# Performance work log

Hardware: AMD Instinct MI355X
Metric: run time of the kernel (lower is better)

The kernel has to match this reference:

```python
import jax, jax.numpy as jnp
import numpy as np

N_NODES = 16384
N_EDGES = 65536
N_GRAPHS = 64


def setup_inputs() -> dict:
    key = jax.random.key(0)
    ks = iter(jax.random.split(key, 64))
    nk = lambda: next(ks)
    p = lambda *s: jax.random.normal(nk(), s, jnp.float32) * 0.1
    inp = {}
    inp['x'] = jax.random.normal(nk(), (N_NODES, 1), jnp.float32)
    inp['edge_index'] = jax.random.randint(nk(), (2, N_EDGES), 0, N_NODES, dtype=jnp.int32)
    inp['batch'] = jnp.sort(jax.random.randint(nk(), (N_NODES,), 0, N_GRAPHS, dtype=jnp.int32))
    for i, (fi, fo) in [(1, (1, 64)), (2, (64, 512)), (3, (512, 2048))]:
        inp[f'gat{i}_wl'] = p(fi, fo)
        inp[f'gat{i}_wr'] = p(fi, fo)
        inp[f'gat{i}_att'] = p(fo)
        inp[f'gat{i}_b'] = jnp.zeros((fo,), jnp.float32)
    for i, c in [(1, 64), (2, 512), (3, 2048), (4, 512), (5, 64)]:
        inp[f'gn{i}_w'] = jnp.ones((c,), jnp.float32)
        inp[f'gn{i}_b'] = jnp.zeros((c,), jnp.float32)
        inp[f'gn{i}_ms'] = jnp.ones((c,), jnp.float32)
    for i, (fi, fo) in [(1, (2048, 512)), (2, (512, 64))]:
        inp[f'arma{i}_wi'] = p(fi, fo)
        inp[f'arma{i}_wr'] = p(fi, fo)
        inp[f'arma{i}_b'] = jnp.zeros((fo,), jnp.float32)
    inp['lin_w'] = p(192, 2)
    inp['lin_b'] = jnp.zeros((2,), jnp.float32)
    return inp


def _seg_softmax(e, idx, n):
    m = jax.ops.segment_max(e, idx, num_segments=n)
    ex = jnp.exp(e - m[idx])
    s = jax.ops.segment_sum(ex, idx, num_segments=n)
    return ex / (s[idx] + 1e-16)


def _gatv2(x, src, dst, wl, wr, att, b):
    # GATv2: e_ij = a^T LeakyReLU(W_l x_j + W_r x_i), softmax over dst neighborhoods
    n = x.shape[0]
    xl = x @ wl
    xr = x @ wr
    e = jax.nn.leaky_relu(xl[src] + xr[dst], 0.2) @ att  # [E]
    a = _seg_softmax(e, dst, n)
    return jax.ops.segment_sum(xl[src] * a[:, None], dst, num_segments=n) + b


def _graph_norm(x, batch, w, b, ms, cnt):
    mean = jax.ops.segment_sum(x, batch, num_segments=N_GRAPHS) / cnt
    out = x - mean[batch] * ms
    var = jax.ops.segment_sum(out * out, batch, num_segments=N_GRAPHS) / cnt
    return w * out / jnp.sqrt(var + 1e-5)[batch] + b


def _arma(x, src, dst, norm, wi, wr, b):
    # ARMAConv, num_stacks=1, num_layers=1: ReLU(Ahat (x Wi) + x Wr + b)
    agg = jax.ops.segment_sum((x @ wi)[src] * norm[:, None], dst, num_segments=x.shape[0])
    return jax.nn.relu(agg + x @ wr + b)


def _forward(x, edge_index, batch,
             gat1_wl, gat1_wr, gat1_att, gat1_b, gn1_w, gn1_b, gn1_ms,
             gat2_wl, gat2_wr, gat2_att, gat2_b, gn2_w, gn2_b, gn2_ms,
             gat3_wl, gat3_wr, gat3_att, gat3_b, gn3_w, gn3_b, gn3_ms,
             arma1_wi, arma1_wr, arma1_b, gn4_w, gn4_b, gn4_ms,
             arma2_wi, arma2_wr, arma2_b, gn5_w, gn5_b, gn5_ms,
             lin_w, lin_b):
    n = x.shape[0]
    src, dst = edge_index[0], edge_index[1]
    sl = jnp.arange(n, dtype=edge_index.dtype)
    src_sl = jnp.concatenate([src, sl])  # GATv2 adds self loops
    dst_sl = jnp.concatenate([dst, sl])
    # gcn_norm without self loops (ARMAConv default)
    deg = jax.ops.segment_sum(jnp.ones_like(src, dtype=x.dtype), dst, num_segments=n)
    dis = jnp.where(deg > 0, 1.0 / jnp.sqrt(jnp.maximum(deg, 1.0)), 0.0)
    norm = dis[src] * dis[dst]
    cnt = jnp.maximum(jax.ops.segment_sum(jnp.ones((n,), x.dtype), batch, num_segments=N_GRAPHS), 1.0)[:, None]

    h = jax.nn.elu(_gatv2(x, src_sl, dst_sl, gat1_wl, gat1_wr, gat1_att, gat1_b))
    h = _graph_norm(h, batch, gn1_w, gn1_b, gn1_ms, cnt)
    h = jax.nn.elu(_gatv2(h, src_sl, dst_sl, gat2_wl, gat2_wr, gat2_att, gat2_b))
    h = _graph_norm(h, batch, gn2_w, gn2_b, gn2_ms, cnt)
    h = jax.nn.elu(_gatv2(h, src_sl, dst_sl, gat3_wl, gat3_wr, gat3_att, gat3_b))
    h = _graph_norm(h, batch, gn3_w, gn3_b, gn3_ms, cnt)
    h = jax.nn.elu(_arma(h, src, dst, norm, arma1_wi, arma1_wr, arma1_b))
    h = _graph_norm(h, batch, gn4_w, gn4_b, gn4_ms, cnt)
    h = jax.nn.elu(_arma(h, src, dst, norm, arma2_wi, arma2_wr, arma2_b))
    h = _graph_norm(h, batch, gn5_w, gn5_b, gn5_ms, cnt)

    x_max = jax.ops.segment_max(h, batch, num_segments=N_GRAPHS)
    x_sum = jax.ops.segment_sum(h, batch, num_segments=N_GRAPHS)
    x_mean = x_sum / cnt
    return jnp.concatenate([x_max, x_mean, x_sum], axis=1) @ lin_w + lin_b


def reference(x, edge_index, batch,
              gat1_wl, gat1_wr, gat1_att, gat1_b, gn1_w, gn1_b, gn1_ms,
              gat2_wl, gat2_wr, gat2_att, gat2_b, gn2_w, gn2_b, gn2_ms,
              gat3_wl, gat3_wr, gat3_att, gat3_b, gn3_w, gn3_b, gn3_ms,
              arma1_wi, arma1_wr, arma1_b, gn4_w, gn4_b, gn4_ms,
              arma2_wi, arma2_wr, arma2_b, gn5_w, gn5_b, gn5_ms,
              lin_w, lin_b):
    return _forward(x, edge_index, batch,
                    gat1_wl, gat1_wr, gat1_att, gat1_b, gn1_w, gn1_b, gn1_ms,
                    gat2_wl, gat2_wr, gat2_att, gat2_b, gn2_w, gn2_b, gn2_ms,
                    gat3_wl, gat3_wr, gat3_att, gat3_b, gn3_w, gn3_b, gn3_ms,
                    arma1_wi, arma1_wr, arma1_b, gn4_w, gn4_b, gn4_ms,
                    arma2_wi, arma2_wr, arma2_b, gn5_w, gn5_b, gn5_ms,
                    lin_w, lin_b)
```

## Files before the change

### kernel.cpp

```cpp
#include <hip/hip_runtime.h>
#include <hip/hip_bf16.h>

#define NN 16384
#define NE 65536
#define NESL (NE + NN)
#define NG 64

typedef __hip_bfloat16 bf16;
typedef __attribute__((ext_vector_type(8))) short short8v;
typedef __attribute__((ext_vector_type(4))) short short4v;
typedef __attribute__((ext_vector_type(4))) float f32x4;
typedef __attribute__((address_space(3))) void lds_void;
typedef const __attribute__((address_space(1))) void glb_void;

__device__ __forceinline__ short bfbits(float v) {
  bf16 h = __float2bfloat16(v);
  return *(short*)&h;
}
__device__ __forceinline__ float bfs2f(short s) {
  return __uint_as_float(((unsigned)(unsigned short)s) << 16);
}
__device__ __forceinline__ void gld16(const void* g, void* l) {
  __builtin_amdgcn_global_load_lds((glb_void*)g, (lds_void*)l, 16, 0, 0);
}

__global__ void k_zero2(int* a, int* b, int n) {
  int i = blockIdx.x * blockDim.x + threadIdx.x;
  if (i < n) { a[i] = 0; b[i] = 0; }
}


__global__ void k_ranges(const int* __restrict__ batch, int* __restrict__ R,
                         float* __restrict__ cnt) {
  int g = threadIdx.x;
  if (g <= NG) {
    int lo = 0, hi = NN;
    while (lo < hi) { int mid = (lo + hi) >> 1; if (batch[mid] < g) lo = mid + 1; else hi = mid; }
    R[g] = lo;
  }
  __syncthreads();
  if (g < NG) cnt[g] = fmaxf((float)(R[g + 1] - R[g]), 1.0f);
}

__global__ void k_deg(const int* __restrict__ dst, int* __restrict__ deg) {
  int e = blockIdx.x * blockDim.x + threadIdx.x;
  if (e < NE) atomicAdd(deg + dst[e], 1);
}

__global__ void k_dis(const int* __restrict__ deg, float* __restrict__ dis) {
  int n = blockIdx.x * blockDim.x + threadIdx.x;
  if (n < NN) { int d = deg[n]; dis[n] = d > 0 ? 1.0f / sqrtf((float)d) : 0.0f; }
}

__global__ void k_scan(const int* __restrict__ deg, int* __restrict__ rowptr) {
  __shared__ int sums[1024];
  int tid = threadIdx.x;
  int base = tid * 16;
  int loc[16];
  int run = 0;
#pragma unroll
  for (int i = 0; i < 16; i++) { run += deg[base + i] + 1; loc[i] = run; }
  sums[tid] = run;
  __syncthreads();
  for (int off = 1; off < 1024; off <<= 1) {
    int v = sums[tid];
    int u = (tid >= off) ? sums[tid - off] : 0;
    __syncthreads();
    sums[tid] = v + u;
    __syncthreads();
  }
  int offset = (tid > 0) ? sums[tid - 1] : 0;
  if (tid == 0) rowptr[0] = 0;
#pragma unroll
  for (int i = 0; i < 16; i++) rowptr[base + i + 1] = loc[i] + offset;
}

__global__ void k_fill(const int* __restrict__ src, const int* __restrict__ dst,
                       const int* __restrict__ rowptr, const float* __restrict__ dis,
                       int* __restrict__ fill, int* __restrict__ srck,
                       float* __restrict__ normk) {
  int e = blockIdx.x * blockDim.x + threadIdx.x;
  if (e >= NESL) return;
  int s = e < NE ? src[e] : e - NE;
  int d = e < NE ? dst[e] : e - NE;
  int pos = rowptr[d] + atomicAdd(fill + d, 1);
  srck[pos] = s;
  normk[pos] = e < NE ? dis[s] * dis[d] : 0.0f;
}

__global__ void k_wsplit2(const float* __restrict__ wa, const float* __restrict__ wb,
                          short* __restrict__ hi, short* __restrict__ lo, int K, int Nw) {
  int gi = blockIdx.x * blockDim.x + threadIdx.x;
  int ngroups = (Nw >> 6) * (K >> 5) * 512;
  if (gi >= ngroups) return;
  int g = gi & 511;
  int t = gi >> 9;
  int nkb = K >> 5;
  int tn = t / nkb, tk = t % nkb;
  int lane = g & 63;
  int n = tn * 128 + ((g >> 6) << 4) + (lane & 15);
  int kb = tk * 32 + ((lane >> 4) << 3);
  const float* w = (n < Nw) ? wa : wb;
  int nn = (n < Nw) ? n : n - Nw;
  short8v h, l;
#pragma unroll
  for (int j = 0; j < 8; j++) {
    float v = w[(size_t)(kb + j) * Nw + nn];
    short hb = bfbits(v);
    h[j] = hb;
    l[j] = bfbits(v - bfs2f(hb));
  }
  *(short8v*)(hi + (size_t)gi * 8) = h;
  *(short8v*)(lo + (size_t)gi * 8) = l;
}

template <int SPLITA, int CBF16, int ACT>
__global__ __launch_bounds__(256) void gemm_mfma_p(const short* __restrict__ Ahi,
                                                   const short* __restrict__ Alo,
                                                   const short* __restrict__ Bthi,
                                                   const short* __restrict__ Btlo,
                                                   void* __restrict__ Cp,
                                                   const float* __restrict__ bias,
                                                   int M, int N, int K) {
  __shared__ __align__(16) short sA[2][(SPLITA ? 2 : 1) * 4096];
  __shared__ __align__(16) short sB[2][8192];
  const int tid = threadIdx.x;
  const int wave = tid >> 6, lane = tid & 63;
  const int wm = wave >> 1, wn = wave & 1;
  const int nbx = gridDim.x;
  const int nwg = nbx * gridDim.y;
  const int hw = blockIdx.y * nbx + blockIdx.x;
  const int lg = (hw & 7) * (nwg >> 3) + (hw >> 3);
  const int row0 = (lg / nbx) * 128, col0 = (lg % nbx) * 128;
  const int nkb = K >> 5;
  const int c = wave * 2;
  const int ar = lane & 15, akc = lane >> 4;
  f32x4 acc[4][4] = {};

  auto stage = [&](int buf, int kb) {
    const short* bh = Bthi + ((size_t)(col0 >> 7) * nkb + kb) * 4096;
    const short* bl = Btlo + ((size_t)(col0 >> 7) * nkb + kb) * 4096;
    gld16(bh + (size_t)c * 512 + lane * 8, (char*)sB[buf] + c * 1024);
    gld16(bh + (size_t)(c + 1) * 512 + lane * 8, (char*)sB[buf] + (c + 1) * 1024);
    gld16(bl + (size_t)c * 512 + lane * 8, (char*)sB[buf] + 8192 + c * 1024);
    gld16(bl + (size_t)(c + 1) * 512 + lane * 8, (char*)sB[buf] + 8192 + (c + 1) * 1024);
    gld16(Ahi + (size_t)(row0 + c * 16 + ar) * K + kb * 32 + akc * 8,
          (char*)sA[buf] + c * 1024);
    gld16(Ahi + (size_t)(row0 + (c + 1) * 16 + ar) * K + kb * 32 + akc * 8,
          (char*)sA[buf] + (c + 1) * 1024);
    if constexpr (SPLITA) {
      gld16(Alo + (size_t)(row0 + c * 16 + ar) * K + kb * 32 + akc * 8,
            (char*)sA[buf] + 8192 + c * 1024);
      gld16(Alo + (size_t)(row0 + (c + 1) * 16 + ar) * K + kb * 32 + akc * 8,
            (char*)sA[buf] + 8192 + (c + 1) * 1024);
    }
  };

  stage(0, 0);
  for (int kb = 0; kb < nkb; kb++) {
    int cur = kb & 1;
    if (kb + 1 < nkb) {
      stage(cur ^ 1, kb + 1);
      if constexpr (SPLITA)
        asm volatile("s_waitcnt vmcnt(8)" ::: "memory");
      else
        asm volatile("s_waitcnt vmcnt(6)" ::: "memory");
    } else {
      asm volatile("s_waitcnt vmcnt(0)" ::: "memory");
    }
    __builtin_amdgcn_sched_barrier(0);
    __builtin_amdgcn_s_barrier();
    __builtin_amdgcn_sched_barrier(0);
    asm volatile("" ::: "memory");
    short8v af[4], al[4], bh[4], bl[4];
#pragma unroll
    for (int f = 0; f < 4; f++) {
      af[f] = *(short8v*)((char*)sA[cur] + (wm * 4 + f) * 1024 + lane * 16);
      if constexpr (SPLITA)
        al[f] = *(short8v*)((char*)sA[cur] + 8192 + (wm * 4 + f) * 1024 + lane * 16);
      bh[f] = *(short8v*)((char*)sB[cur] + (wn * 4 + f) * 1024 + lane * 16);
      bl[f] = *(short8v*)((char*)sB[cur] + 8192 + (wn * 4 + f) * 1024 + lane * 16);
    }
#pragma unroll
    for (int i = 0; i < 4; i++)
#pragma unroll
      for (int j = 0; j < 4; j++) {
        acc[i][j] = __builtin_amdgcn_mfma_f32_16x16x32_bf16(af[i], bh[j], acc[i][j], 0, 0, 0);
        acc[i][j] = __builtin_amdgcn_mfma_f32_16x16x32_bf16(af[i], bl[j], acc[i][j], 0, 0, 0);
        if constexpr (SPLITA)
          acc[i][j] = __builtin_amdgcn_mfma_f32_16x16x32_bf16(al[i], bh[j], acc[i][j], 0, 0, 0);
      }
    asm volatile("" ::: "memory");
    __builtin_amdgcn_sched_barrier(0);
    __builtin_amdgcn_s_barrier();
    __builtin_amdgcn_sched_barrier(0);
  }
#pragma unroll
  for (int i = 0; i < 4; i++)
#pragma unroll
    for (int j = 0; j < 4; j++)
#pragma unroll
      for (int r = 0; r < 4; r++) {
        int row = row0 + wm * 64 + i * 16 + ((lane >> 4) << 2) + r;
        int col = col0 + wn * 64 + j * 16 + (lane & 15);
        float v = acc[i][j][r];
        if (bias) v += bias[col];
        if constexpr (ACT == 1) v = v > 0.0f ? v : expf(v) - 1.0f;
        if constexpr (ACT == 2) v = fmaxf(v, 0.0f);
        if constexpr (CBF16) {
          ((short*)Cp)[(size_t)row * N + col] = bfbits(v);
        } else {
          ((float*)Cp)[(size_t)row * N + col] = v;
        }
      }
}

__global__ void k_gat1_csr(const float* __restrict__ x, const float* __restrict__ wl,
                           const float* __restrict__ wr, const float* __restrict__ att,
                           const int* __restrict__ rowptr, const int* __restrict__ srck,
                           float* __restrict__ ework, const float* __restrict__ bias,
                           float* __restrict__ out) {
  int node = blockIdx.x * 4 + (threadIdx.x >> 6);
  int lane = threadIdx.x & 63;
  float wlv = wl[lane], wrv = wr[lane], av = att[lane];
  float xd = x[node];
  int beg = rowptr[node], end = rowptr[node + 1];
  float m = -INFINITY;
  for (int k = beg; k < end; k++) {
    float v = x[srck[k]] * wlv + xd * wrv;
    v = v > 0.0f ? v : 0.2f * v;
    float e = av * v;
#pragma unroll
    for (int off = 32; off; off >>= 1) e += __shfl_xor(e, off);
    if (lane == 0) ework[k] = e;
    m = fmaxf(m, e);
  }
  __syncthreads();
  float sum = 0.0f, agg = 0.0f;
  for (int k = beg + lane; k < end; k += 64) {
    float p = expf(ework[k] - m);
    sum += p;
    agg += p * x[srck[k]];
  }
#pragma unroll
  for (int off = 32; off; off >>= 1) {
    sum += __shfl_xor(sum, off);
    agg += __shfl_xor(agg, off);
  }
  float o = agg / (sum + 1e-16f) * wlv + bias[lane];
  out[(size_t)node * 64 + lane] = o > 0.0f ? o : expf(o) - 1.0f;
}

template <int FO, int STR, typename XT>
__global__ void k_logits_csr(const XT* __restrict__ X, const float* __restrict__ att,
                             const int* __restrict__ rowptr, const int* __restrict__ srck,
                             float* __restrict__ pk, float* __restrict__ ssum) {
  int node = blockIdx.x * 4 + (threadIdx.x >> 6);
  int lane = threadIdx.x & 63;
  constexpr int NV = FO / 64;
  float xr[NV], at[NV];
  if constexpr (sizeof(XT) == 2) {
    const short* xrp = (const short*)X + (size_t)node * STR + FO;
#pragma unroll
    for (int j = 0; j < FO / 512; j++) {
      short8v v = *(const short8v*)(xrp + j * 512 + lane * 8);
      f32x4 a0 = *(const f32x4*)(att + j * 512 + lane * 8);
      f32x4 a1 = *(const f32x4*)(att + j * 512 + lane * 8 + 4);
#pragma unroll
      for (int t = 0; t < 8; t++) {
        xr[j * 8 + t] = bfs2f(v[t]);
        at[j * 8 + t] = t < 4 ? a0[t] : a1[t - 4];
      }
    }
  } else {
    const float* xrp = (const float*)X + (size_t)node * STR + FO;
#pragma unroll
    for (int j = 0; j < FO / 256; j++) {
      f32x4 v = *(const f32x4*)(xrp + j * 256 + lane * 4);
      f32x4 a = *(const f32x4*)(att + j * 256 + lane * 4);
#pragma unroll
      for (int t = 0; t < 4; t++) {
        xr[j * 4 + t] = v[t];
        at[j * 4 + t] = a[t];
      }
    }
  }
  int beg = rowptr[node], end = rowptr[node + 1];
  float m = -INFINITY;
  for (int k = beg; k < end; k++) {
    int s = srck[k];
    float acc = 0.0f;
    if constexpr (sizeof(XT) == 2) {
      const short* xlp = (const short*)X + (size_t)s * STR;
#pragma unroll
      for (int j = 0; j < FO / 512; j++) {
        short8v v = *(const short8v*)(xlp + j * 512 + lane * 8);
#pragma unroll
        for (int t = 0; t < 8; t++) {
          float u = bfs2f(v[t]) + xr[j * 8 + t];
          u = u > 0.0f ? u : 0.2f * u;
          acc += at[j * 8 + t] * u;
        }
      }
    } else {
      const float* xlp = (const float*)X + (size_t)s * STR;
#pragma unroll
      for (int j = 0; j < FO / 256; j++) {
        f32x4 v = *(const f32x4*)(xlp + j * 256 + lane * 4);
#pragma unroll
        for (int t = 0; t < 4; t++) {
          float u = v[t] + xr[j * 4 + t];
          u = u > 0.0f ? u : 0.2f * u;
          acc += at[j * 4 + t] * u;
        }
      }
    }
#pragma unroll
    for (int off = 32; off; off >>= 1) acc += __shfl_xor(acc, off);
    if (lane == 0) pk[k] = acc;
    m = fmaxf(m, acc);
  }
  __syncthreads();
  float sum = 0.0f;
  for (int k = beg + lane; k < end; k += 64) {
    float p = expf(pk[k] - m);
    pk[k] = p;
    sum += p;
  }
#pragma unroll
  for (int off = 32; off; off >>= 1) sum += __shfl_xor(sum, off);
  if (lane == 0) ssum[node] = sum;
}

template <int MODE, int SSTR, int OSTR>
__global__ void k_agg512(const float* __restrict__ Xsrc, const float* __restrict__ pk,
                         const float* __restrict__ ssum, const int* __restrict__ rowptr,
                         const int* __restrict__ srck, const float* __restrict__ normk,
                         const float* __restrict__ xwrb, const float* __restrict__ bias,
                         float* __restrict__ out, short* __restrict__ outhi,
                         short* __restrict__ outlo) {
  int wave = threadIdx.x >> 6;
  int node = blockIdx.x * 2 + (wave >> 1);
  int lane = threadIdx.x & 63;
  int c0 = (wave & 1) * 256 + lane * 4;
  f32x4 acc = {};
  int beg = rowptr[node], end = rowptr[node + 1];
  float inv = (MODE == 0) ? 1.0f / (ssum[node] + 1e-16f) : 1.0f;
  for (int k = beg; k < end; k++) {
    int s = srck[k];
    float w = (MODE == 0) ? pk[k] * inv : normk[k];
    f32x4 v = *(const f32x4*)(Xsrc + (size_t)s * SSTR + c0);
#pragma unroll
    for (int t = 0; t < 4; t++) acc[t] += w * v[t];
  }
  if constexpr (MODE == 1) {
    f32x4 xv = *(const f32x4*)(xwrb + (size_t)node * SSTR + 512 + c0);
#pragma unroll
    for (int t = 0; t < 4; t++) acc[t] = fmaxf(acc[t] + xv[t] + bias[c0 + t], 0.0f);
    *(f32x4*)(out + (size_t)node * OSTR + c0) = acc;
  } else {
    short4v hh, ll;
#pragma unroll
    for (int t = 0; t < 4; t++) {
      hh[t] = bfbits(acc[t]);
      ll[t] = bfbits(acc[t] - bfs2f(hh[t]));
    }
    *(short4v*)(outhi + (size_t)node * OSTR + c0) = hh;
    *(short4v*)(outlo + (size_t)node * OSTR + c0) = ll;
  }
}

template <int MODE, int SSTR, int XOFF>
__global__ void k_agg64(const float* __restrict__ Xsrc, const float* __restrict__ pk,
                        const float* __restrict__ ssum, const int* __restrict__ rowptr,
                        const int* __restrict__ srck, const float* __restrict__ normk,
                        const float* __restrict__ xwrb, const float* __restrict__ bias,
                        float* __restrict__ out, short* __restrict__ outhi,
                        short* __restrict__ outlo) {
  int node = blockIdx.x * (blockDim.x >> 6) + (threadIdx.x >> 6);
  if (node >= NN) return;
  int lane = threadIdx.x & 63;
  int cg = lane & 15, eg = lane >> 4;
  int c0 = cg * 4;
  f32x4 acc = {};
  int beg = rowptr[node], end = rowptr[node + 1];
  float inv = (MODE == 0) ? 1.0f / (ssum[node] + 1e-16f) : 1.0f;
  for (int k = beg + eg; k < end; k += 4) {
    int s = srck[k];
    float w = (MODE == 0) ? pk[k] * inv : normk[k];
    f32x4 v = *(const f32x4*)(Xsrc + (size_t)s * SSTR + c0);
#pragma unroll
    for (int t = 0; t < 4; t++) acc[t] += w * v[t];
  }
#pragma unroll
  for (int t = 0; t < 4; t++) {
    acc[t] += __shfl_xor(acc[t], 16);
    acc[t] += __shfl_xor(acc[t], 32);
  }
  if (eg == 0) {
    if constexpr (MODE == 1) {
      f32x4 xv = *(const f32x4*)(xwrb + (size_t)node * SSTR + XOFF + c0);
#pragma unroll
      for (int t = 0; t < 4; t++) acc[t] = fmaxf(acc[t] + xv[t] + bias[c0 + t], 0.0f);
      *(f32x4*)(out + (size_t)node * 64 + c0) = acc;
    } else {
      short4v hh, ll;
#pragma unroll
      for (int t = 0; t < 4; t++) {
        hh[t] = bfbits(acc[t]);
        ll[t] = bfbits(acc[t] - bfs2f(hh[t]));
      }
      *(short4v*)(outhi + (size_t)node * 64 + c0) = hh;
      *(short4v*)(outlo + (size_t)node * 64 + c0) = ll;
    }
  }
}

template <typename T, int VEC>
__global__ void k_gn_stats_v(const T* __restrict__ x, const int* __restrict__ R, int C,
                             float* __restrict__ s1, float* __restrict__ s2) {
  int g = blockIdx.x;
  int c0 = (blockIdx.y * blockDim.x + threadIdx.x) * VEC;
  if (c0 >= C) return;
  int beg = R[g], end = R[g + 1];
  float a[VEC] = {}, b[VEC] = {};
  for (int n = beg; n < end; n++) {
    const T* p = x + (size_t)n * C + c0;
    float v[VEC];
    if constexpr (sizeof(T) == 2) {
      short8v h = *(const short8v*)p;
#pragma unroll
      for (int t = 0; t < VEC; t++) v[t] = bfs2f(h[t]);
    } else {
      f32x4 h = *(const f32x4*)p;
#pragma unroll
      for (int t = 0; t < VEC; t++) v[t] = h[t];
    }
#pragma unroll
    for (int t = 0; t < VEC; t++) {
      a[t] += v[t];
      b[t] += v[t] * v[t];
    }
  }
#pragma unroll
  for (int t = 0; t < VEC; t++) {
    s1[g * C + c0 + t] = a[t];
    s2[g * C + c0 + t] = b[t];
  }
}

template <typename T, int VEC, int EMIT>
__global__ void k_gn_apply_v(T* __restrict__ x, const int* __restrict__ batch,
                             const float* __restrict__ cnt, const float* __restrict__ s1,
                             const float* __restrict__ s2, const float* __restrict__ w,
                             const float* __restrict__ b, const float* __restrict__ ms, int C,
                             int total_vec, short* __restrict__ hip,
                             short* __restrict__ lop) {
  int i = blockIdx.x * blockDim.x + threadIdx.x;
  if (i >= total_vec) return;
  int cpv = C / VEC;
  int n = i / cpv, c0 = (i % cpv) * VEC;
  int g = batch[n];
  float ct = cnt[g];
  T* p = x + (size_t)n * C + c0;
  float v[VEC];
  if constexpr (sizeof(T) == 2) {
    short8v h = *(const short8v*)p;
#pragma unroll
    for (int t = 0; t < VEC; t++) v[t] = bfs2f(h[t]);
  } else {
    f32x4 h = *(const f32x4*)p;
#pragma unroll
    for (int t = 0; t < VEC; t++) v[t] = h[t];
  }
#pragma unroll
  for (int t = 0; t < VEC; t++) {
    int cc = c0 + t;
    float mean = s1[g * C + cc] / ct;
    float mm = mean * ms[cc];
    float var = s2[g * C + cc] / ct - 2.0f * mm * mean + mm * mm;
    v[t] = (v[t] - mm) * (1.0f / sqrtf(var + 1e-5f)) * w[cc] + b[cc];
  }
  if constexpr (sizeof(T) == 2) {
    short8v h;
#pragma unroll
    for (int t = 0; t < VEC; t++) h[t] = bfbits(v[t]);
    *(short8v*)p = h;
  } else {
    f32x4 h;
#pragma unroll
    for (int t = 0; t < VEC; t++) h[t] = v[t];
    *(f32x4*)p = h;
  }
  if constexpr (EMIT >= 2) {
    short4v hh;
#pragma unroll
    for (int t = 0; t < VEC; t++) hh[t] = bfbits(v[t]);
    *(short4v*)(hip + (size_t)n * C + c0) = hh;
    if constexpr (EMIT == 3) {
      short4v ll;
#pragma unroll
      for (int t = 0; t < VEC; t++) ll[t] = bfbits(v[t] - bfs2f(hh[t]));
      *(short4v*)(lop + (size_t)n * C + c0) = ll;
    }
  }
}

__global__ void k_pool(const float* __restrict__ h, const int* __restrict__ R,
                       const float* __restrict__ cnt, const float* __restrict__ lw,
                       const float* __restrict__ lb, float* __restrict__ out) {
  int g = blockIdx.x;
  int c = threadIdx.x;
  int beg = R[g], end = R[g + 1];
  float mx = -INFINITY, sm = 0.0f;
  for (int n = beg; n < end; n++) {
    float v = h[(size_t)n * 64 + c];
    mx = fmaxf(mx, v);
    sm += v;
  }
  __shared__ float feat[192];
  feat[c] = mx;
  feat[64 + c] = sm / cnt[g];
  feat[128 + c] = sm;
  __syncthreads();
  if (c < 2) {
    float acc = lb[c];
    for (int j = 0; j < 192; j++) acc += feat[j] * lw[j * 2 + c];
    out[g * 2 + c] = acc;
  }
}


extern "C" void kernel_launch(void* const* d_in, const int* in_sizes, int n_in,
                              void* d_out, int out_size, void* d_ws, size_t ws_size,
                              hipStream_t stream) {
  const float* x = (const float*)d_in[0];
  const int* ei = (const int*)d_in[1];
  const int* batch = (const int*)d_in[2];
  const float* g1wl = (const float*)d_in[3];
  const float* g1wr = (const float*)d_in[4];
  const float* g1att = (const float*)d_in[5];
  const float* g1b = (const float*)d_in[6];
  const float* g2wl = (const float*)d_in[7];
  const float* g2wr = (const float*)d_in[8];
  const float* g2att = (const float*)d_in[9];
  const float* g2b = (const float*)d_in[10];
  const float* g3wl = (const float*)d_in[11];
  const float* g3wr = (const float*)d_in[12];
  const float* g3att = (const float*)d_in[13];
  const float* g3b = (const float*)d_in[14];
  const float* gn1w = (const float*)d_in[15];
  const float* gn1b = (const float*)d_in[16];
  const float* gn1ms = (const float*)d_in[17];
  const float* gn2w = (const float*)d_in[18];
  const float* gn2b = (const float*)d_in[19];
  const float* gn2ms = (const float*)d_in[20];
  const float* gn3w = (const float*)d_in[21];
  const float* gn3b = (const float*)d_in[22];
  const float* gn3ms = (const float*)d_in[23];
  const float* gn4w = (const float*)d_in[24];
  const float* gn4b = (const float*)d_in[25];
  const float* gn4ms = (const float*)d_in[26];
  const float* gn5w = (const float*)d_in[27];
  const float* gn5b = (const float*)d_in[28];
  const float* gn5ms = (const float*)d_in[29];
  const float* a1wi = (const float*)d_in[30];
  const float* a1wr = (const float*)d_in[31];
  const float* a1b = (const float*)d_in[32];
  const float* a2wi = (const float*)d_in[33];
  const float* a2wr = (const float*)d_in[34];
  const float* a2b = (const float*)d_in[35];
  const float* linw = (const float*)d_in[36];
  const float* linb = (const float*)d_in[37];
  const int* srcp = ei;
  const int* dstp = ei + NE;
  float* out = (float*)d_out;

  float* ws = (float*)d_ws;
  size_t o = 0;
  auto alloc = [&](size_t nfloats) { float* p = ws + o; o += nfloats; return p; };
  float* BIG0f = alloc((size_t)NN * 1024);
  float* BIG1f = alloc((size_t)NN * 1024);
  float* B0 = alloc((size_t)NN * 512);
  float* B1 = alloc((size_t)NN * 512);
  float* h1 = alloc((size_t)NN * 64);
  float* S0 = alloc((size_t)NN * 64);
  float* S1 = alloc((size_t)NN * 64);
  float* S2 = alloc((size_t)NN * 64);
  float* pk = alloc(NESL);
  float* normk = alloc(NESL);
  float* ssum = alloc(NN);
  float* dis = alloc(NN);
  float* cnt = alloc(NG);
  float* s1 = alloc(NG * 2048);
  float* s2 = alloc(NG * 2048);
  short* WThi = (short*)alloc((size_t)4096 * 512 / 2);
  short* WTlo = (short*)alloc((size_t)4096 * 512 / 2);
  int* deg = (int*)alloc(NN);
  int* rowptr = (int*)alloc(NN + 1);
  int* fill = (int*)alloc(NN);
  int* srck = (int*)alloc(NESL);
  int* R = (int*)alloc(72);

  bf16* XLR3 = (bf16*)BIG0f;
  bf16* h3 = (bf16*)BIG0f;
  float* h4 = BIG1f;
  short* h4hi = (short*)BIG0f;
  short* h4lo = h4hi + (size_t)NN * 512;
  short* XLR2 = (short*)B0;
  float* h2 = B0;
  short* h2hi = (short*)B1;
  short* agg2hi = (short*)B1;
  short* agg2lo = agg2hi + (size_t)NN * 512;
  float* TXW1 = B0;
  float* TXW2 = S0;
  short* h1hi = (short*)S2;
  short* h1lo = h1hi + (size_t)NN * 64;
  short* aggShi = (short*)S0;
  short* aggSlo = aggShi + (size_t)NN * 64;
  float* h5 = S2;

  k_zero2<<<NN / 256, 256, 0, stream>>>(deg, fill, NN);
  k_ranges<<<1, 128, 0, stream>>>(batch, R, cnt);
  k_deg<<<NE / 256, 256, 0, stream>>>(dstp, deg);
  k_scan<<<1, 1024, 0, stream>>>(deg, rowptr);
  k_dis<<<NN / 256, 256, 0, stream>>>(deg, dis);
  k_fill<<<(NESL + 255) / 256, 256, 0, stream>>>(srcp, dstp, rowptr, dis, fill, srck, normk);

  k_gat1_csr<<<NN / 4, 256, 0, stream>>>(x, g1wl, g1wr, g1att, rowptr, srck, pk, g1b, h1);
  k_gn_stats_v<float, 4><<<dim3(NG, 1), 16, 0, stream>>>(h1, R, 64, s1, s2);
  k_gn_apply_v<float, 4, 3><<<NN * 16 / 256, 256, 0, stream>>>(h1, batch, cnt, s1, s2, gn1w,
                                                               gn1b, gn1ms, 64, NN * 16, h1hi,
                                                               h1lo);

  k_wsplit2<<<8192 / 256, 256, 0, stream>>>(g2wl, g2wr, WThi, WTlo, 64, 512);
  gemm_mfma_p<1, 1, 0><<<dim3(8, 128), 256, 0, stream>>>(h1hi, h1lo, WThi, WTlo, XLR2, nullptr,
                                                         NN, 1024, 64);
  k_logits_csr<512, 1024, bf16><<<NN / 4, 256, 0, stream>>>((const bf16*)XLR2, g2att, rowptr,
                                                            srck, pk, ssum);
  k_agg64<0, 64, 0><<<NN / 4, 256, 0, stream>>>(h1, pk, ssum, rowptr, srck, normk, nullptr,
                                                nullptr, nullptr, aggShi, aggSlo);
  gemm_mfma_p<1, 0, 1><<<dim3(4, 128), 256, 0, stream>>>(aggShi, aggSlo, WThi, WTlo, h2, g2b,
                                                         NN, 512, 64);
  k_gn_stats_v<float, 4><<<dim3(NG, 1), 128, 0, stream>>>(h2, R, 512, s1, s2);
  k_gn_apply_v<float, 4, 2><<<NN * 128 / 256, 256, 0, stream>>>(h2, batch, cnt, s1, s2, gn2w,
                                                                gn2b, gn2ms, 512, NN * 128,
                                                                h2hi, nullptr);

  k_wsplit2<<<262144 / 256, 256, 0, stream>>>(g3wl, g3wr, WThi, WTlo, 512, 2048);
  gemm_mfma_p<0, 1, 0><<<dim3(32, 128), 256, 0, stream>>>(h2hi, nullptr, WThi, WTlo, XLR3,
                                                          nullptr, NN, 4096, 512);
  k_logits_csr<2048, 4096, bf16><<<NN / 4, 256, 0, stream>>>(XLR3, g3att, rowptr, srck, pk, ssum);
  k_agg512<0, 512, 512><<<NN / 2, 256, 0, stream>>>(h2, pk, ssum, rowptr, srck, normk, nullptr,
                                                    nullptr, nullptr, agg2hi, agg2lo);
  gemm_mfma_p<1, 1, 1><<<dim3(16, 128), 256, 0, stream>>>(agg2hi, agg2lo, WThi, WTlo, h3, g3b,
                                                          NN, 2048, 512);
  k_gn_stats_v<bf16, 8><<<dim3(NG, 1), 256, 0, stream>>>(h3, R, 2048, s1, s2);
  k_gn_apply_v<bf16, 8, 0><<<NN * 256 / 256, 256, 0, stream>>>(h3, batch, cnt, s1, s2, gn3w,
                                                               gn3b, gn3ms, 2048, NN * 256,
                                                               nullptr, nullptr);

  k_wsplit2<<<262144 / 256, 256, 0, stream>>>(a1wi, a1wr, WThi, WTlo, 2048, 512);
  gemm_mfma_p<0, 0, 0><<<dim3(8, 128), 256, 0, stream>>>((const short*)h3, nullptr, WThi, WTlo,
                                                         TXW1, nullptr, NN, 1024, 2048);
  k_agg512<1, 1024, 512><<<NN / 2, 256, 0, stream>>>(TXW1, pk, nullptr, rowptr, srck, normk,
                                                     TXW1, a1b, h4, nullptr, nullptr);
  k_gn_stats_v<float, 4><<<dim3(NG, 1), 128, 0, stream>>>(h4, R, 512, s1, s2);
  k_gn_apply_v<float, 4, 3><<<NN * 128 / 256, 256, 0, stream>>>(h4, batch, cnt, s1, s2, gn4w,
                                                                gn4b, gn4ms, 512, NN * 128,
                                                                h4hi, h4lo);

  k_wsplit2<<<8192 / 256, 256, 0, stream>>>(a2wi, a2wr, WThi, WTlo, 512, 64);
  gemm_mfma_p<1, 0, 0><<<dim3(1, 128), 256, 0, stream>>>(h4hi, h4lo, WThi, WTlo, TXW2, nullptr,
                                                         NN, 128, 512);
  k_agg64<1, 128, 64><<<NN / 4, 256, 0, stream>>>(TXW2, pk, nullptr, rowptr, srck, normk, TXW2,
                                                  a2b, h5, nullptr, nullptr);
  k_gn_stats_v<float, 4><<<dim3(NG, 1), 16, 0, stream>>>(h5, R, 64, s1, s2);
  k_gn_apply_v<float, 4, 0><<<NN * 16 / 256, 256, 0, stream>>>(h5, batch, cnt, s1, s2, gn5w,
                                                               gn5b, gn5ms, 64, NN * 16, nullptr,
                                                               nullptr);

  k_pool<<<NG, 64, 0, stream>>>(h5, R, cnt, linw, linb, out);
}
```

Measured before the change: 1.279 ms.

## Add 256-row GEMM tile variant and split graph-norm stats over row chunks

```diff
diff --git a/kernel.cpp b/kernel.cpp
--- a/kernel.cpp
+++ b/kernel.cpp
@@ -215,6 +215,98 @@
       }
 }
 
+template <int CBF16, int ACT>
+__global__ __launch_bounds__(512) void gemm_mfma_p256(const short* __restrict__ Ahi,
+                                                      const short* __restrict__ Bthi,
+                                                      const short* __restrict__ Btlo,
+                                                      void* __restrict__ Cp,
+                                                      const float* __restrict__ bias,
+                                                      int M, int N, int K) {
+  __shared__ __align__(16) short sA[2][8192];
+  __shared__ __align__(16) short sB[2][8192];
+  const int tid = threadIdx.x;
+  const int wave = tid >> 6, lane = tid & 63;
+  const int wm = wave >> 1, wn = wave & 1;
+  const int nbx = gridDim.x;
+  const int nwg = nbx * gridDim.y;
+  const int hw = blockIdx.y * nbx + blockIdx.x;
+  const int lg = (hw & 7) * (nwg >> 3) + (hw >> 3);
+  const int row0 = (lg / nbx) * 256, col0 = (lg % nbx) * 128;
+  const int nkb = K >> 5;
+  const int ar = lane & 15, akc = lane >> 4;
+  f32x4 acc[4][4] = {};
+
+  auto stage = [&](int buf, int kb) {
+    if (wave < 4) {
+      const short* bh = Bthi + ((size_t)(col0 >> 7) * nkb + kb) * 4096;
+      int cB = wave * 2;
+      gld16(bh + (size_t)cB * 512 + lane * 8, (char*)sB[buf] + cB * 1024);
+      gld16(bh + (size_t)(cB + 1) * 512 + lane * 8, (char*)sB[buf] + (cB + 1) * 1024);
+    } else {
+      const short* bl = Btlo + ((size_t)(col0 >> 7) * nkb + kb) * 4096;
+      int cB = (wave - 4) * 2;
+      gld16(bl + (size_t)cB * 512 + lane * 8, (char*)sB[buf] + 8192 + cB * 1024);
+      gld16(bl + (size_t)(cB + 1) * 512 + lane * 8, (char*)sB[buf] + 8192 + (cB + 1) * 1024);
+    }
+    int cA = wave * 2;
+    gld16(Ahi + (size_t)(row0 + cA * 16 + ar) * K + kb * 32 + akc * 8,
+          (char*)sA[buf] + cA * 1024);
+    gld16(Ahi + (size_t)(row0 + (cA + 1) * 16 + ar) * K + kb * 32 + akc * 8,
+          (char*)sA[buf] + (cA + 1) * 1024);
+  };
+
+  stage(0, 0);
+  for (int kb = 0; kb < nkb; kb++) {
+    int cur = kb & 1;
+    if (kb + 1 < nkb) {
+      stage(cur ^ 1, kb + 1);
+      asm volatile("s_waitcnt vmcnt(4)" ::: "memory");
+    } else {
+      asm volatile("s_waitcnt vmcnt(0)" ::: "memory");
+    }
+    __builtin_amdgcn_sched_barrier(0);
+    __builtin_amdgcn_s_barrier();
+    __builtin_amdgcn_sched_barrier(0);
+    asm volatile("" ::: "memory");
+    short8v af[4], bh[4], bl[4];
+#pragma unroll
+    for (int f = 0; f < 4; f++) {
+      af[f] = *(short8v*)((char*)sA[cur] + (wm * 4 + f) * 1024 + lane * 16);
+      bh[f] = *(short8v*)((char*)sB[cur] + (wn * 4 + f) * 1024 + lane * 16);
+      bl[f] = *(short8v*)((char*)sB[cur] + 8192 + (wn * 4 + f) * 1024 + lane * 16);
+    }
+#pragma unroll
+    for (int i = 0; i < 4; i++)
+#pragma unroll
+      for (int j = 0; j < 4; j++) {
+        acc[i][j] = __builtin_amdgcn_mfma_f32_16x16x32_bf16(af[i], bh[j], acc[i][j], 0, 0, 0);
+        acc[i][j] = __builtin_amdgcn_mfma_f32_16x16x32_bf16(af[i], bl[j], acc[i][j], 0, 0, 0);
+      }
+    asm volatile("" ::: "memory");
+    __builtin_amdgcn_sched_barrier(0);
+    __builtin_amdgcn_s_barrier();
+    __builtin_amdgcn_sched_barrier(0);
+  }
+#pragma unroll
+  for (int i = 0; i < 4; i++)
+#pragma unroll
+    for (int j = 0; j < 4; j++)
+#pragma unroll
+      for (int r = 0; r < 4; r++) {
+        int row = row0 + wm * 64 + i * 16 + ((lane >> 4) << 2) + r;
+        int col = col0 + wn * 64 + j * 16 + (lane & 15);
+        float v = acc[i][j][r];
+        if (bias) v += bias[col];
+        if constexpr (ACT == 1) v = v > 0.0f ? v : expf(v) - 1.0f;
+        if constexpr (ACT == 2) v = fmaxf(v, 0.0f);
+        if constexpr (CBF16) {
+          ((short*)Cp)[(size_t)row * N + col] = bfbits(v);
+        } else {
+          ((float*)Cp)[(size_t)row * N + col] = v;
+        }
+      }
+}
+
 __global__ void k_gat1_csr(const float* __restrict__ x, const float* __restrict__ wl,
                            const float* __restrict__ wr, const float* __restrict__ att,
                            const int* __restrict__ rowptr, const int* __restrict__ srck,
@@ -418,13 +510,18 @@
 
 template <typename T, int VEC>
 __global__ void k_gn_stats_v(const T* __restrict__ x, const int* __restrict__ R, int C,
-                             float* __restrict__ s1, float* __restrict__ s2) {
+                             float* __restrict__ s1p, float* __restrict__ s2p) {
   int g = blockIdx.x;
-  int c0 = (blockIdx.y * blockDim.x + threadIdx.x) * VEC;
+  int rs = blockIdx.y;
+  int RS = gridDim.y;
+  int c0 = threadIdx.x * VEC;
   if (c0 >= C) return;
   int beg = R[g], end = R[g + 1];
+  int len = end - beg;
+  int lo = beg + (int)(((long long)len * rs) / RS);
+  int hi2 = beg + (int)(((long long)len * (rs + 1)) / RS);
   float a[VEC] = {}, b[VEC] = {};
-  for (int n = beg; n < end; n++) {
+  for (int n = lo; n < hi2; n++) {
     const T* p = x + (size_t)n * C + c0;
     float v[VEC];
     if constexpr (sizeof(T) == 2) {
@@ -444,15 +541,15 @@
   }
 #pragma unroll
   for (int t = 0; t < VEC; t++) {
-    s1[g * C + c0 + t] = a[t];
-    s2[g * C + c0 + t] = b[t];
+    s1p[((size_t)rs * NG + g) * C + c0 + t] = a[t];
+    s2p[((size_t)rs * NG + g) * C + c0 + t] = b[t];
   }
 }
 
 template <typename T, int VEC, int EMIT>
 __global__ void k_gn_apply_v(T* __restrict__ x, const int* __restrict__ batch,
-                             const float* __restrict__ cnt, const float* __restrict__ s1,
-                             const float* __restrict__ s2, const float* __restrict__ w,
+                             const float* __restrict__ cnt, const float* __restrict__ s1p,
+                             const float* __restrict__ s2p, const float* __restrict__ w,
                              const float* __restrict__ b, const float* __restrict__ ms, int C,
                              int total_vec, short* __restrict__ hip,
                              short* __restrict__ lop) {
@@ -476,9 +573,15 @@
 #pragma unroll
   for (int t = 0; t < VEC; t++) {
     int cc = c0 + t;
-    float mean = s1[g * C + cc] / ct;
+    float sv1 = 0.0f, sv2 = 0.0f;
+#pragma unroll
+    for (int rs = 0; rs < 4; rs++) {
+      sv1 += s1p[((size_t)rs * NG + g) * C + cc];
+      sv2 += s2p[((size_t)rs * NG + g) * C + cc];
+    }
+    float mean = sv1 / ct;
     float mm = mean * ms[cc];
-    float var = s2[g * C + cc] / ct - 2.0f * mm * mean + mm * mm;
+    float var = sv2 / ct - 2.0f * mm * mean + mm * mm;
     v[t] = (v[t] - mm) * (1.0f / sqrtf(var + 1e-5f)) * w[cc] + b[cc];
   }
   if constexpr (sizeof(T) == 2) {
@@ -592,8 +695,8 @@
   float* ssum = alloc(NN);
   float* dis = alloc(NN);
   float* cnt = alloc(NG);
-  float* s1 = alloc(NG * 2048);
-  float* s2 = alloc(NG * 2048);
+  float* s1 = alloc((size_t)4 * NG * 2048);
+  float* s2 = alloc((size_t)4 * NG * 2048);
   short* WThi = (short*)alloc((size_t)4096 * 512 / 2);
   short* WTlo = (short*)alloc((size_t)4096 * 512 / 2);
   int* deg = (int*)alloc(NN);
@@ -628,7 +731,7 @@
   k_fill<<<(NESL + 255) / 256, 256, 0, stream>>>(srcp, dstp, rowptr, dis, fill, srck, normk);
 
   k_gat1_csr<<<NN / 4, 256, 0, stream>>>(x, g1wl, g1wr, g1att, rowptr, srck, pk, g1b, h1);
-  k_gn_stats_v<float, 4><<<dim3(NG, 1), 16, 0, stream>>>(h1, R, 64, s1, s2);
+  k_gn_stats_v<float, 4><<<dim3(NG, 4), 16, 0, stream>>>(h1, R, 64, s1, s2);
   k_gn_apply_v<float, 4, 3><<<NN * 16 / 256, 256, 0, stream>>>(h1, batch, cnt, s1, s2, gn1w,
                                                                gn1b, gn1ms, 64, NN * 16, h1hi,
                                                                h1lo);
@@ -642,30 +745,30 @@
                                                 nullptr, nullptr, aggShi, aggSlo);
   gemm_mfma_p<1, 0, 1><<<dim3(4, 128), 256, 0, stream>>>(aggShi, aggSlo, WThi, WTlo, h2, g2b,
                                                          NN, 512, 64);
-  k_gn_stats_v<float, 4><<<dim3(NG, 1), 128, 0, stream>>>(h2, R, 512, s1, s2);
+  k_gn_stats_v<float, 4><<<dim3(NG, 4), 128, 0, stream>>>(h2, R, 512, s1, s2);
   k_gn_apply_v<float, 4, 2><<<NN * 128 / 256, 256, 0, stream>>>(h2, batch, cnt, s1, s2, gn2w,
                                                                 gn2b, gn2ms, 512, NN * 128,
                                                                 h2hi, nullptr);
 
   k_wsplit2<<<262144 / 256, 256, 0, stream>>>(g3wl, g3wr, WThi, WTlo, 512, 2048);
-  gemm_mfma_p<0, 1, 0><<<dim3(32, 128), 256, 0, stream>>>(h2hi, nullptr, WThi, WTlo, XLR3,
-                                                          nullptr, NN, 4096, 512);
+  gemm_mfma_p256<1, 0><<<dim3(32, 64), 512, 0, stream>>>(h2hi, WThi, WTlo, XLR3, nullptr, NN,
+                                                         4096, 512);
   k_logits_csr<2048, 4096, bf16><<<NN / 4, 256, 0, stream>>>(XLR3, g3att, rowptr, srck, pk, ssum);
   k_agg512<0, 512, 512><<<NN / 2, 256, 0, stream>>>(h2, pk, ssum, rowptr, srck, normk, nullptr,
                                                     nullptr, nullptr, agg2hi, agg2lo);
   gemm_mfma_p<1, 1, 1><<<dim3(16, 128), 256, 0, stream>>>(agg2hi, agg2lo, WThi, WTlo, h3, g3b,
                                                           NN, 2048, 512);
-  k_gn_stats_v<bf16, 8><<<dim3(NG, 1), 256, 0, stream>>>(h3, R, 2048, s1, s2);
+  k_gn_stats_v<bf16, 8><<<dim3(NG, 4), 256, 0, stream>>>(h3, R, 2048, s1, s2);
   k_gn_apply_v<bf16, 8, 0><<<NN * 256 / 256, 256, 0, stream>>>(h3, batch, cnt, s1, s2, gn3w,
                                                                gn3b, gn3ms, 2048, NN * 256,
                                                                nullptr, nullptr);
 
   k_wsplit2<<<262144 / 256, 256, 0, stream>>>(a1wi, a1wr, WThi, WTlo, 2048, 512);
-  gemm_mfma_p<0, 0, 0><<<dim3(8, 128), 256, 0, stream>>>((const short*)h3, nullptr, WThi, WTlo,
-                                                         TXW1, nullptr, NN, 1024, 2048);
+  gemm_mfma_p256<0, 0><<<dim3(8, 64), 512, 0, stream>>>((const short*)h3, WThi, WTlo, TXW1,
+                                                        nullptr, NN, 1024, 2048);
   k_agg512<1, 1024, 512><<<NN / 2, 256, 0, stream>>>(TXW1, pk, nullptr, rowptr, srck, normk,
                                                      TXW1, a1b, h4, nullptr, nullptr);
-  k_gn_stats_v<float, 4><<<dim3(NG, 1), 128, 0, stream>>>(h4, R, 512, s1, s2);
+  k_gn_stats_v<float, 4><<<dim3(NG, 4), 128, 0, stream>>>(h4, R, 512, s1, s2);
   k_gn_apply_v<float, 4, 3><<<NN * 128 / 256, 256, 0, stream>>>(h4, batch, cnt, s1, s2, gn4w,
                                                                 gn4b, gn4ms, 512, NN * 128,
                                                                 h4hi, h4lo);
@@ -675,7 +778,7 @@
                                                          NN, 128, 512);
   k_agg64<1, 128, 64><<<NN / 4, 256, 0, stream>>>(TXW2, pk, nullptr, rowptr, srck, normk, TXW2,
                                                   a2b, h5, nullptr, nullptr);
-  k_gn_stats_v<float, 4><<<dim3(NG, 1), 16, 0, stream>>>(h5, R, 64, s1, s2);
+  k_gn_stats_v<float, 4><<<dim3(NG, 4), 16, 0, stream>>>(h5, R, 64, s1, s2);
   k_gn_apply_v<float, 4, 0><<<NN * 16 / 256, 256, 0, stream>>>(h5, batch, cnt, s1, s2, gn5w,
                                                                gn5b, gn5ms, 64, NN * 16, nullptr,
                                                                nullptr);
```

New measurement: 1.102 ms. -13.9%, faster.
